# Performance work log

Hardware: AMD Instinct MI355X
Metric: run time of the kernel (lower is better)

## Reference

```python
import jax, jax.numpy as jnp
import numpy as np

ALPHA = 300.0   # attractor_alpha
N_ATT = 16      # n_attractors
MIN_D = 0.001
MAX_D = 10.0


def _resize_bilinear_ac(x, out_h, out_w):
    """Bilinear resize with align_corners=True on trailing (H, W) dims of [B,C,h,w]."""
    h, w = x.shape[-2], x.shape[-1]
    ys = jnp.arange(out_h, dtype=jnp.float32) * ((h - 1) / max(out_h - 1, 1))
    xs = jnp.arange(out_w, dtype=jnp.float32) * ((w - 1) / max(out_w - 1, 1))
    y0 = jnp.floor(ys).astype(jnp.int32); y1 = jnp.minimum(y0 + 1, h - 1)
    x0 = jnp.floor(xs).astype(jnp.int32); x1 = jnp.minimum(x0 + 1, w - 1)
    wy = (ys - y0.astype(jnp.float32))[:, None]   # [out_h, 1]
    wx = (xs - x0.astype(jnp.float32))[None, :]   # [1, out_w]
    v00 = x[..., y0[:, None], x0[None, :]]
    v01 = x[..., y0[:, None], x1[None, :]]
    v10 = x[..., y1[:, None], x0[None, :]]
    v11 = x[..., y1[:, None], x1[None, :]]
    top = v00 * (1 - wx) + v01 * wx
    bot = v10 * (1 - wx) + v11 * wx
    return top * (1 - wy) + bot * wy


def setup_inputs() -> dict:
    key = jax.random.key(0)
    k = jax.random.split(key, 7)
    B, C, H, W = 4, 128, 192, 192
    n_bins = 64
    x = jax.random.normal(k[0], (B, C, H, W), dtype=jnp.float32)
    prev_bin = jax.random.uniform(k[1], (B, n_bins, H // 2, W // 2), dtype=jnp.float32)
    prev_bin_embedding = jax.random.normal(k[2], (B, C, H // 2, W // 2), dtype=jnp.float32)
    w1 = jax.random.normal(k[3], (128, 128), dtype=jnp.float32) * 0.05
    b1 = jnp.zeros((128,), dtype=jnp.float32)
    w2 = jax.random.normal(k[4], (2 * N_ATT, 128), dtype=jnp.float32) * 0.05
    b2 = jnp.zeros((2 * N_ATT,), dtype=jnp.float32)
    return {"x": x, "prev_bin": prev_bin, "prev_bin_embedding": prev_bin_embedding,
            "w1": w1, "b1": b1, "w2": w2, "b2": b2}


def reference(x, prev_bin, prev_bin_embedding, w1, b1, w2, b2):
    B, C, H, W = x.shape
    # add (interpolated) previous bin embedding
    pe = _resize_bilinear_ac(prev_bin_embedding, H, W)
    h = x + pe
    # per-pixel MLP (two 1x1 convs)
    h = jax.nn.relu(jnp.einsum('bchw,oc->bohw', h, w1) + b1[:, None, None])
    att = jax.nn.relu(jnp.einsum('bchw,oc->bohw', h, w2) + b2[:, None, None]) + 0.001
    # [B, n_attractors, 2, H, W] -> take normed attractor points
    att = att.reshape(B, N_ATT, 2, H, W)[:, :, 0]          # [B, nA, H, W]
    # upsample previous bin centers to feature resolution
    bc = _resize_bilinear_ac(prev_bin, H, W)               # [B, nB, H, W]
    # broadcast-subtract + inverse attractor + mean over attractors
    dx = att[:, :, None, :, :] - bc[:, None, :, :, :]      # [B, nA, nB, H, W]
    delta_c = jnp.mean(dx / (1.0 + ALPHA * dx * dx), axis=1)  # gamma = 2
    bin_new_centers = bc + delta_c
    bin_centers = (MAX_D - MIN_D) * bin_new_centers + MIN_D
    bin_centers = jnp.clip(jnp.sort(bin_centers, axis=1), MIN_D, MAX_D)
    return bin_new_centers, bin_centers
```

## Files before the change

kernel.cpp:

```cpp
#include <hip/hip_runtime.h>

constexpr int Bc = 4, Cc = 128, Hc = 192, Wc = 192;
constexpr int HI = 96, WI = 96;
constexpr int NB = 64;
constexpr int NA = 16;
constexpr float SCL = 95.0f / 191.0f;

typedef __attribute__((ext_vector_type(8))) short bf16x8;
typedef __attribute__((ext_vector_type(4))) float f32x4;

__device__ __forceinline__ unsigned short f2bf(float f) {
  unsigned u = __builtin_bit_cast(unsigned, f);
  unsigned r = (u + 0x7FFFu + ((u >> 16) & 1u)) >> 16;
  return (unsigned short)r;
}
__device__ __forceinline__ float rcp_fast(float r) {
#if defined(__has_builtin)
#if __has_builtin(__builtin_amdgcn_rcpf)
  return __builtin_amdgcn_rcpf(r);
#else
  return 1.0f / r;
#endif
#else
  return 1.0f / r;
#endif
}

__global__ __launch_bounds__(256) void k_prep(
    const float* __restrict__ w1, const float* __restrict__ w2,
    unsigned short* __restrict__ w1p, unsigned short* __restrict__ w2p)
{
  const int t = blockIdx.x * 256 + threadIdx.x;
  if (t < 16384) {
    const int e  = t & 7;
    const int l  = (t >> 3) & 63;
    const int kt = (t >> 9) & 3;
    const int nt = t >> 11;
    const int n  = nt * 16 + (l & 15);
    const int k  = kt * 32 + (l >> 4) * 8 + e;
    w1p[t] = f2bf(w1[n * 128 + k]);
  } else {
    const int u  = t - 16384;
    const int e  = u & 7;
    const int l  = (u >> 3) & 63;
    const int kt = u >> 9;
    const int n  = 2 * (l & 15);
    const int k  = kt * 32 + (l >> 4) * 8 + e;
    w2p[u] = f2bf(w2[n * 128 + k]);
  }
}

__global__ __launch_bounds__(256, 3) void k_att(
    const float* __restrict__ x, const float* __restrict__ pbe,
    const unsigned short* __restrict__ w1p, const float* __restrict__ b1,
    const unsigned short* __restrict__ w2p, const float* __restrict__ b2,
    float* __restrict__ att)
{
  constexpr int PH = 136;
  constexpr int RP = 37;
  __shared__ __align__(16) unsigned char smem[32768 + 128 * RP * 4];
  unsigned short* w1_s  = (unsigned short*)smem;
  float*          row_s = (float*)(smem + 32768);
  unsigned short* a1_s  = (unsigned short*)(smem + 32768);

  const int tid = threadIdx.x;
  const int xg0 = blockIdx.x * 64;
  const int y = blockIdx.y;
  const int b = blockIdx.z;

  const float ysf = y * SCL;
  const int y0 = (int)ysf;
  const int y1 = min(y0 + 1, HI - 1);
  const float wy = ysf - (float)y0;
  const int xi0 = (int)(xg0 * SCL);

  const int lane = tid & 63;
  const int wv = tid >> 6;
  const int ln = lane & 15;
  const int qd = lane >> 4;
  const int m0 = wv * 16;

  const int px = m0 + ln;
  const int xg = xg0 + px;
  const float xsf = (float)xg * SCL;
  const int x0i = (int)xsf;
  const float wx = xsf - (float)x0i;
  const int xl = x0i - xi0;

  float4 wstage[8];
  {
    const float4* wp4 = (const float4*)w1p;
    #pragma unroll
    for (int i = 0; i < 8; ++i) wstage[i] = wp4[tid + 256 * i];
  }

  bf16x8 b2f[4];
  #pragma unroll
  for (int kt = 0; kt < 4; ++kt)
    b2f[kt] = *(const bf16x8*)&w2p[kt * 512 + lane * 8];
  float bias1[8];
  #pragma unroll
  for (int nt = 0; nt < 8; ++nt) bias1[nt] = b1[nt * 16 + ln];
  const float bias2 = b2[2 * ln];

  float xr[32];
  #pragma unroll
  for (int kt = 0; kt < 4; ++kt) {
    #pragma unroll
    for (int j = 0; j < 8; ++j) {
      const int c = kt * 32 + qd * 8 + j;
      xr[kt * 8 + j] = x[((size_t)(b * Cc + c) * Hc + y) * Wc + xg];
    }
  }

  #pragma unroll
  for (int i = 0; i < 18; ++i) {
    const int f = tid + 256 * i;
    const int c = f / 36;
    const int xi = f - c * 36;
    const int xgl = min(xi0 + xi, WI - 1);
    const float* p = pbe + (size_t)(b * Cc + c) * (HI * WI);
    const float top = p[y0 * WI + xgl];
    const float bot = p[y1 * WI + xgl];
    row_s[c * RP + xi] = top + wy * (bot - top);
  }

  {
    float4* ws4 = (float4*)w1_s;
    #pragma unroll
    for (int i = 0; i < 8; ++i) ws4[tid + 256 * i] = wstage[i];
  }
  __syncthreads();

  bf16x8 af[4];
  #pragma unroll
  for (int kt = 0; kt < 4; ++kt) {
    #pragma unroll
    for (int j = 0; j < 8; ++j) {
      const int c = kt * 32 + qd * 8 + j;
      const float v0 = row_s[c * RP + xl];
      const float v1 = row_s[c * RP + xl + 1];
      af[kt][j] = (short)f2bf(xr[kt * 8 + j] + v0 + wx * (v1 - v0));
    }
  }
  __syncthreads();

  f32x4 acc[8];
  #pragma unroll
  for (int nt = 0; nt < 8; ++nt) acc[nt] = f32x4{0.f, 0.f, 0.f, 0.f};
  #pragma unroll
  for (int nt = 0; nt < 8; ++nt) {
    #pragma unroll
    for (int kt = 0; kt < 4; ++kt) {
      const bf16x8 bf = *(const bf16x8*)&w1_s[(nt * 4 + kt) * 512 + lane * 8];
      acc[nt] = __builtin_amdgcn_mfma_f32_16x16x32_bf16(af[kt], bf, acc[nt], 0, 0, 0);
    }
  }

  #pragma unroll
  for (int nt = 0; nt < 8; ++nt) {
    const int n = nt * 16 + ln;
    const float bias = bias1[nt];
    #pragma unroll
    for (int r = 0; r < 4; ++r) {
      const int m = m0 + qd * 4 + r;
      a1_s[m * PH + n] = f2bf(fmaxf(acc[nt][r] + bias, 0.f));
    }
  }

  f32x4 acc2 = f32x4{0.f, 0.f, 0.f, 0.f};
  #pragma unroll
  for (int kt = 0; kt < 4; ++kt) {
    const bf16x8 a2 = *(const bf16x8*)&a1_s[(m0 + ln) * PH + kt * 32 + qd * 8];
    acc2 = __builtin_amdgcn_mfma_f32_16x16x32_bf16(a2, b2f[kt], acc2, 0, 0, 0);
  }
  #pragma unroll
  for (int r = 0; r < 4; ++r) {
    const int opx = m0 + qd * 4 + r;
    const float v = fmaxf(acc2[r] + bias2, 0.f) + 0.001f;
    att[((size_t)((b * Hc + y) * Wc) + xg0 + opx) * NA + ln] = v;
  }
}

__global__ __launch_bounds__(384, 4) void k_bins(
    const float* __restrict__ pb, const float* __restrict__ att,
    float* __restrict__ out0, float* __restrict__ out1)
{
  __shared__ __align__(16) float row_s[NB][WI];
  float* xch = &row_s[0][0];

  const int tid = threadIdx.x;
  const int h = (tid >= 192) ? 1 : 0;
  const int px = tid - 192 * h;
  const int y = blockIdx.x;
  const int b = blockIdx.y;

  const float ysf = y * SCL;
  const int y0 = (int)ysf;
  const int y1 = min(y0 + 1, HI - 1);
  const float wy = ysf - (float)y0;

  float am[16];
  {
    const float4* ap = (const float4*)(att + ((size_t)((b * Hc + y) * Wc) + px) * NA);
    const float4 a0 = ap[0], a1 = ap[1], a2 = ap[2], a3 = ap[3];
    am[0] = a0.x;  am[1] = a0.y;  am[2] = a0.z;  am[3] = a0.w;
    am[4] = a1.x;  am[5] = a1.y;  am[6] = a1.z;  am[7] = a1.w;
    am[8] = a2.x;  am[9] = a2.y;  am[10] = a2.z; am[11] = a2.w;
    am[12] = a3.x; am[13] = a3.y; am[14] = a3.z; am[15] = a3.w;
  }

  #pragma unroll
  for (int i = 0; i < 4; ++i) {
    const int u = tid + 384 * i;
    const int k = u / 24;
    const int g = u - k * 24;
    const float* base = pb + (size_t)(b * NB + k) * (HI * WI);
    const float4 t4 = *(const float4*)&base[y0 * WI + g * 4];
    const float4 b4 = *(const float4*)&base[y1 * WI + g * 4];
    float4 r;
    r.x = t4.x + wy * (b4.x - t4.x);
    r.y = t4.y + wy * (b4.y - t4.y);
    r.z = t4.z + wy * (b4.z - t4.z);
    r.w = t4.w + wy * (b4.w - t4.w);
    *(float4*)&row_s[k][g * 4] = r;
  }
  __syncthreads();

  const float xsf = px * SCL;
  const int x0 = (int)xsf;
  const float wx = xsf - (float)x0;

  const size_t obase = (size_t)(b * NB) * (Hc * Wc) + (size_t)y * Wc + px;
  float v[32];

  #pragma unroll
  for (int kb = 0; kb < 32; kb += 4) {
    float bc[4], dl[4];
    #pragma unroll
    for (int q = 0; q < 4; ++q) {
      const int k = h * 32 + kb + q;
      const float v0 = row_s[k][x0], v1 = row_s[k][x0 + 1];
      bc[q] = v0 + wx * (v1 - v0);
      dl[q] = 0.f;
    }
    #pragma unroll
    for (int j = 0; j < NA; ++j) {
      const float a = am[j];
      #pragma unroll
      for (int q = 0; q < 4; ++q) {
        const float d = a - bc[q];
        const float rq = fmaf(300.f * d, d, 1.f);
        dl[q] = fmaf(d, rcp_fast(rq), dl[q]);
      }
    }
    #pragma unroll
    for (int q = 0; q < 4; ++q) {
      const float bnc = fmaf(dl[q], 1.f / 16.f, bc[q]);
      out0[obase + (size_t)(h * 32 + kb + q) * (Hc * Wc)] = bnc;
      v[kb + q] = fmaf(9.999f, bnc, 0.001f);
    }
  }

  if (h == 0) {
    #pragma unroll
    for (int size = 2; size <= 32; size <<= 1)
      #pragma unroll
      for (int stride = size >> 1; stride >= 1; stride >>= 1)
        #pragma unroll
        for (int i = 0; i < 32; ++i)
          if ((i & stride) == 0) {
            const int j = i | stride;
            const bool asc = ((i & size) == 0);
            const float a = v[i], c = v[j];
            const float lo = fminf(a, c), hi = fmaxf(a, c);
            v[i] = asc ? lo : hi;
            v[j] = asc ? hi : lo;
          }
  } else {
    #pragma unroll
    for (int size = 2; size <= 32; size <<= 1)
      #pragma unroll
      for (int stride = size >> 1; stride >= 1; stride >>= 1)
        #pragma unroll
        for (int i = 0; i < 32; ++i)
          if ((i & stride) == 0) {
            const int j = i | stride;
            const bool asc = ((i & size) != 0);
            const float a = v[i], c = v[j];
            const float lo = fminf(a, c), hi = fmaxf(a, c);
            v[i] = asc ? lo : hi;
            v[j] = asc ? hi : lo;
          }
  }

  __syncthreads();
  if (h) {
    #pragma unroll
    for (int i = 0; i < 32; ++i) xch[i * 192 + px] = v[i];
  }
  __syncthreads();
  if (!h) {
    #pragma unroll
    for (int i = 0; i < 32; ++i) {
      const float o = xch[i * 192 + px];
      const float mn = fminf(v[i], o), mx = fmaxf(v[i], o);
      v[i] = mn;
      xch[i * 192 + px] = mx;
    }
  }
  __syncthreads();
  if (h) {
    #pragma unroll
    for (int i = 0; i < 32; ++i) v[i] = xch[i * 192 + px];
  }

  #pragma unroll
  for (int stride = 16; stride >= 1; stride >>= 1)
    #pragma unroll
    for (int i = 0; i < 32; ++i)
      if ((i & stride) == 0) {
        const int j = i | stride;
        const float a = v[i], c = v[j];
        v[i] = fminf(a, c);
        v[j] = fmaxf(a, c);
      }

  #pragma unroll
  for (int i = 0; i < 32; ++i) {
    out1[obase + (size_t)(h * 32 + i) * (Hc * Wc)] =
        fminf(fmaxf(v[i], 0.001f), 10.0f);
  }
}

extern "C" void kernel_launch(void* const* d_in, const int* in_sizes, int n_in,
                              void* d_out, int out_size, void* d_ws, size_t ws_size,
                              hipStream_t stream) {
  const float* x   = (const float*)d_in[0];
  const float* pb  = (const float*)d_in[1];
  const float* pbe = (const float*)d_in[2];
  const float* w1  = (const float*)d_in[3];
  const float* b1  = (const float*)d_in[4];
  const float* w2  = (const float*)d_in[5];
  const float* b2  = (const float*)d_in[6];

  float* out0 = (float*)d_out;
  float* out1 = out0 + (size_t)Bc * NB * Hc * Wc;

  unsigned short* w1p = (unsigned short*)d_ws;
  unsigned short* w2p = w1p + 16384;
  float* att = (float*)((char*)d_ws + 65536);

  k_prep<<<72, 256, 0, stream>>>(w1, w2, w1p, w2p);

  dim3 g1(Wc / 64, Hc, Bc);
  k_att<<<g1, 256, 0, stream>>>(x, pbe, w1p, b1, w2p, b2, att);

  dim3 g2(Hc, Bc);
  k_bins<<<g2, 384, 0, stream>>>(pb, att, out0, out1);
}
```

Before: 213.0 us.

## Fuse attractor MLP and bin-center kernels into one per-row kernel

Merges the attractor MLP kernel and the bin update kernel into a single kernel with one 384-thread block per image row. Attractor values now stay in shared memory instead of being written to and read back from a global workspace. The block covers the full row, so the interpolated embedding row is staged once in shared memory with an XOR swizzle to avoid bank conflicts. The trade-offs are a large 80KB shared allocation that limits occupancy, fewer blocks overall (768), and the MLP and bin phases running serially inside each block.

```diff
diff --git a/kernel.cpp b/kernel.cpp
--- a/kernel.cpp
+++ b/kernel.cpp
@@ -50,48 +50,44 @@
   }
 }
 
-__global__ __launch_bounds__(256, 3) void k_att(
+__global__ __launch_bounds__(384, 3) void k_row(
     const float* __restrict__ x, const float* __restrict__ pbe,
     const unsigned short* __restrict__ w1p, const float* __restrict__ b1,
     const unsigned short* __restrict__ w2p, const float* __restrict__ b2,
-    float* __restrict__ att)
+    const float* __restrict__ pb,
+    float* __restrict__ out0, float* __restrict__ out1)
 {
-  constexpr int PH = 136;
-  constexpr int RP = 37;
-  __shared__ __align__(16) unsigned char smem[32768 + 128 * RP * 4];
+  __shared__ __align__(16) unsigned char smem[81920];
   unsigned short* w1_s  = (unsigned short*)smem;
   float*          row_s = (float*)(smem + 32768);
-  unsigned short* a1_s  = (unsigned short*)(smem + 32768);
+  unsigned short* a1_b  = (unsigned short*)(smem + 32768);
+  float*          att_s = (float*)(smem + 58880);
+  float*          pbrow = (float*)smem;
+  float*          xch   = (float*)(smem + 24576);
 
   const int tid = threadIdx.x;
-  const int xg0 = blockIdx.x * 64;
-  const int y = blockIdx.y;
-  const int b = blockIdx.z;
+  const int y = blockIdx.x;
+  const int b = blockIdx.y;
+
+  const int lane = tid & 63;
+  const int wv = tid >> 6;
+  const int ln = lane & 15;
+  const int qd = lane >> 4;
 
   const float ysf = y * SCL;
   const int y0 = (int)ysf;
   const int y1 = min(y0 + 1, HI - 1);
   const float wy = ysf - (float)y0;
-  const int xi0 = (int)(xg0 * SCL);
-
-  const int lane = tid & 63;
-  const int wv = tid >> 6;
-  const int ln = lane & 15;
-  const int qd = lane >> 4;
-  const int m0 = wv * 16;
-
-  const int px = m0 + ln;
-  const int xg = xg0 + px;
-  const float xsf = (float)xg * SCL;
-  const int x0i = (int)xsf;
-  const float wx = xsf - (float)x0i;
-  const int xl = x0i - xi0;
-
-  float4 wstage[8];
+
+
+  float4 wstage[6];
   {
     const float4* wp4 = (const float4*)w1p;
     #pragma unroll
-    for (int i = 0; i < 8; ++i) wstage[i] = wp4[tid + 256 * i];
+    for (int i = 0; i < 6; ++i) {
+      const int u = tid + 384 * i;
+      wstage[i] = (u < 2048) ? wp4[u] : float4{0.f, 0.f, 0.f, 0.f};
+    }
   }
 
   bf16x8 b2f[4];
@@ -103,111 +99,114 @@
   for (int nt = 0; nt < 8; ++nt) bias1[nt] = b1[nt * 16 + ln];
   const float bias2 = b2[2 * ln];
 
-  float xr[32];
-  #pragma unroll
-  for (int kt = 0; kt < 4; ++kt) {
-    #pragma unroll
-    for (int j = 0; j < 8; ++j) {
-      const int c = kt * 32 + qd * 8 + j;
-      xr[kt * 8 + j] = x[((size_t)(b * Cc + c) * Hc + y) * Wc + xg];
-    }
-  }
-
-  #pragma unroll
-  for (int i = 0; i < 18; ++i) {
-    const int f = tid + 256 * i;
-    const int c = f / 36;
-    const int xi = f - c * 36;
-    const int xgl = min(xi0 + xi, WI - 1);
+  float xr[2][32];
+  #pragma unroll
+  for (int mt = 0; mt < 2; ++mt) {
+    const int px = wv * 32 + mt * 16 + ln;
+    #pragma unroll
+    for (int kt = 0; kt < 4; ++kt) {
+      #pragma unroll
+      for (int j = 0; j < 8; ++j) {
+        const int c = kt * 32 + qd * 8 + j;
+        xr[mt][kt * 8 + j] = x[((size_t)(b * Cc + c) * Hc + y) * Wc + px];
+      }
+    }
+  }
+
+  #pragma unroll
+  for (int i = 0; i < 32; ++i) {
+    const int f = tid + 384 * i;
+    const int c = f / 96;
+    const int xi = f - c * 96;
     const float* p = pbe + (size_t)(b * Cc + c) * (HI * WI);
-    const float top = p[y0 * WI + xgl];
-    const float bot = p[y1 * WI + xgl];
-    row_s[c * RP + xi] = top + wy * (bot - top);
+    const float top = p[y0 * WI + xi];
+    const float bot = p[y1 * WI + xi];
+    row_s[c * 96 + (xi ^ ((((c >> 3) & 3)) << 3))] = top + wy * (bot - top);
   }
 
   {
     float4* ws4 = (float4*)w1_s;
     #pragma unroll
-    for (int i = 0; i < 8; ++i) ws4[tid + 256 * i] = wstage[i];
-  }
-  __syncthreads();
-
-  bf16x8 af[4];
-  #pragma unroll
-  for (int kt = 0; kt < 4; ++kt) {
-    #pragma unroll
-    for (int j = 0; j < 8; ++j) {
-      const int c = kt * 32 + qd * 8 + j;
-      const float v0 = row_s[c * RP + xl];
-      const float v1 = row_s[c * RP + xl + 1];
-      af[kt][j] = (short)f2bf(xr[kt * 8 + j] + v0 + wx * (v1 - v0));
-    }
-  }
-  __syncthreads();
-
-  f32x4 acc[8];
-  #pragma unroll
-  for (int nt = 0; nt < 8; ++nt) acc[nt] = f32x4{0.f, 0.f, 0.f, 0.f};
-  #pragma unroll
-  for (int nt = 0; nt < 8; ++nt) {
+    for (int i = 0; i < 6; ++i) {
+      const int u = tid + 384 * i;
+      if (u < 2048) ws4[u] = wstage[i];
+    }
+  }
+  __syncthreads();
+
+  bf16x8 af[2][4];
+  const int sw = qd << 3;
+  #pragma unroll
+  for (int mt = 0; mt < 2; ++mt) {
+    const int px = wv * 32 + mt * 16 + ln;
+    const float xsf = (float)px * SCL;
+    const int xl = (int)xsf;
+    const float wx = xsf - (float)xl;
+    const int i0 = xl ^ sw;
+    const int i1 = (xl + 1) ^ sw;
     #pragma unroll
     for (int kt = 0; kt < 4; ++kt) {
-      const bf16x8 bf = *(const bf16x8*)&w1_s[(nt * 4 + kt) * 512 + lane * 8];
-      acc[nt] = __builtin_amdgcn_mfma_f32_16x16x32_bf16(af[kt], bf, acc[nt], 0, 0, 0);
-    }
-  }
-
-  #pragma unroll
-  for (int nt = 0; nt < 8; ++nt) {
-    const int n = nt * 16 + ln;
-    const float bias = bias1[nt];
+      #pragma unroll
+      for (int j = 0; j < 8; ++j) {
+        const int c = kt * 32 + qd * 8 + j;
+        const float v0 = row_s[c * 96 + i0];
+        const float v1 = row_s[c * 96 + i1];
+        af[mt][kt][j] = (short)f2bf(xr[mt][kt * 8 + j] + v0 + wx * (v1 - v0));
+      }
+    }
+  }
+  __syncthreads();
+
+  unsigned short* a1w = a1_b + wv * (16 * 136);
+
+  #pragma unroll
+  for (int mt = 0; mt < 2; ++mt) {
+    f32x4 acc[8];
+    #pragma unroll
+    for (int nt = 0; nt < 8; ++nt) acc[nt] = f32x4{0.f, 0.f, 0.f, 0.f};
+    #pragma unroll
+    for (int nt = 0; nt < 8; ++nt) {
+      #pragma unroll
+      for (int kt = 0; kt < 4; ++kt) {
+        const bf16x8 bf = *(const bf16x8*)&w1_s[(nt * 4 + kt) * 512 + lane * 8];
+        acc[nt] = __builtin_amdgcn_mfma_f32_16x16x32_bf16(af[mt][kt], bf, acc[nt], 0, 0, 0);
+      }
+    }
+    #pragma unroll
+    for (int nt = 0; nt < 8; ++nt) {
+      const int n = nt * 16 + ln;
+      const float bias = bias1[nt];
+      #pragma unroll
+      for (int r = 0; r < 4; ++r) {
+        a1w[(qd * 4 + r) * 136 + n] = f2bf(fmaxf(acc[nt][r] + bias, 0.f));
+      }
+    }
+    f32x4 acc2 = f32x4{0.f, 0.f, 0.f, 0.f};
+    #pragma unroll
+    for (int kt = 0; kt < 4; ++kt) {
+      const bf16x8 a2 = *(const bf16x8*)&a1w[ln * 136 + kt * 32 + qd * 8];
+      acc2 = __builtin_amdgcn_mfma_f32_16x16x32_bf16(a2, b2f[kt], acc2, 0, 0, 0);
+    }
     #pragma unroll
     for (int r = 0; r < 4; ++r) {
-      const int m = m0 + qd * 4 + r;
-      a1_s[m * PH + n] = f2bf(fmaxf(acc[nt][r] + bias, 0.f));
-    }
-  }
-
-  f32x4 acc2 = f32x4{0.f, 0.f, 0.f, 0.f};
-  #pragma unroll
-  for (int kt = 0; kt < 4; ++kt) {
-    const bf16x8 a2 = *(const bf16x8*)&a1_s[(m0 + ln) * PH + kt * 32 + qd * 8];
-    acc2 = __builtin_amdgcn_mfma_f32_16x16x32_bf16(a2, b2f[kt], acc2, 0, 0, 0);
-  }
-  #pragma unroll
-  for (int r = 0; r < 4; ++r) {
-    const int opx = m0 + qd * 4 + r;
-    const float v = fmaxf(acc2[r] + bias2, 0.f) + 0.001f;
-    att[((size_t)((b * Hc + y) * Wc) + xg0 + opx) * NA + ln] = v;
-  }
-}
-
-__global__ __launch_bounds__(384, 4) void k_bins(
-    const float* __restrict__ pb, const float* __restrict__ att,
-    float* __restrict__ out0, float* __restrict__ out1)
-{
-  __shared__ __align__(16) float row_s[NB][WI];
-  float* xch = &row_s[0][0];
-
-  const int tid = threadIdx.x;
+      const int opx = wv * 32 + mt * 16 + qd * 4 + r;
+      att_s[opx * 20 + ln] = fmaxf(acc2[r] + bias2, 0.f) + 0.001f;
+    }
+  }
+  __syncthreads();
+
+
   const int h = (tid >= 192) ? 1 : 0;
   const int px = tid - 192 * h;
-  const int y = blockIdx.x;
-  const int b = blockIdx.y;
-
-  const float ysf = y * SCL;
-  const int y0 = (int)ysf;
-  const int y1 = min(y0 + 1, HI - 1);
-  const float wy = ysf - (float)y0;
 
   float am[16];
   {
-    const float4* ap = (const float4*)(att + ((size_t)((b * Hc + y) * Wc) + px) * NA);
-    const float4 a0 = ap[0], a1 = ap[1], a2 = ap[2], a3 = ap[3];
-    am[0] = a0.x;  am[1] = a0.y;  am[2] = a0.z;  am[3] = a0.w;
-    am[4] = a1.x;  am[5] = a1.y;  am[6] = a1.z;  am[7] = a1.w;
-    am[8] = a2.x;  am[9] = a2.y;  am[10] = a2.z; am[11] = a2.w;
-    am[12] = a3.x; am[13] = a3.y; am[14] = a3.z; am[15] = a3.w;
+    const f32x4* ap = (const f32x4*)&att_s[px * 20];
+    const f32x4 a0 = ap[0], a1 = ap[1], a2 = ap[2], a3 = ap[3];
+    am[0] = a0[0];  am[1] = a0[1];  am[2] = a0[2];  am[3] = a0[3];
+    am[4] = a1[0];  am[5] = a1[1];  am[6] = a1[2];  am[7] = a1[3];
+    am[8] = a2[0];  am[9] = a2[1];  am[10] = a2[2]; am[11] = a2[3];
+    am[12] = a3[0]; am[13] = a3[1]; am[14] = a3[2]; am[15] = a3[3];
   }
 
   #pragma unroll
@@ -223,7 +222,7 @@
     r.y = t4.y + wy * (b4.y - t4.y);
     r.z = t4.z + wy * (b4.z - t4.z);
     r.w = t4.w + wy * (b4.w - t4.w);
-    *(float4*)&row_s[k][g * 4] = r;
+    *(float4*)&pbrow[k * 96 + g * 4] = r;
   }
   __syncthreads();
 
@@ -240,7 +239,7 @@
     #pragma unroll
     for (int q = 0; q < 4; ++q) {
       const int k = h * 32 + kb + q;
-      const float v0 = row_s[k][x0], v1 = row_s[k][x0 + 1];
+      const float v0 = pbrow[k * 96 + x0], v1 = pbrow[k * 96 + x0 + 1];
       bc[q] = v0 + wx * (v1 - v0);
       dl[q] = 0.f;
     }
@@ -349,13 +348,9 @@
 
   unsigned short* w1p = (unsigned short*)d_ws;
   unsigned short* w2p = w1p + 16384;
-  float* att = (float*)((char*)d_ws + 65536);
 
   k_prep<<<72, 256, 0, stream>>>(w1, w2, w1p, w2p);
 
-  dim3 g1(Wc / 64, Hc, Bc);
-  k_att<<<g1, 256, 0, stream>>>(x, pbe, w1p, b1, w2p, b2, att);
-
-  dim3 g2(Hc, Bc);
-  k_bins<<<g2, 384, 0, stream>>>(pb, att, out0, out1);
-}
+  dim3 g(Hc, Bc);
+  k_row<<<g, 384, 0, stream>>>(x, pbe, w1p, b1, w2p, b2, pb, out0, out1);
+}
```

New measurement: 265.7 us. 1.25x slower.

## Halve k_att weight staging in LDS and split k_bins rows across two blocks

Applied to the files above, without the earlier changes.

k_att now loads the first-layer weights into shared memory in two halves. The first half is used for four output tiles, then overwritten with the second half. This halves the weight buffer and raises the launch-bounds occupancy target from 3 to 4 blocks, at the cost of an extra barrier and more phases. k_bins now splits each row into two 192-thread blocks, each covering 96 pixels with a narrower padded interpolation buffer. This gives more, smaller blocks for better SM fill and lower LDS use per block. The bitonic sort's two direction branches are merged into one loop with a direction predicate.

```diff
diff --git a/kernel.cpp b/kernel.cpp
--- a/kernel.cpp
+++ b/kernel.cpp
@@ -50,7 +50,7 @@
   }
 }
 
-__global__ __launch_bounds__(256, 3) void k_att(
+__global__ __launch_bounds__(256, 4) void k_att(
     const float* __restrict__ x, const float* __restrict__ pbe,
     const unsigned short* __restrict__ w1p, const float* __restrict__ b1,
     const unsigned short* __restrict__ w2p, const float* __restrict__ b2,
@@ -58,10 +58,10 @@
 {
   constexpr int PH = 136;
   constexpr int RP = 37;
-  __shared__ __align__(16) unsigned char smem[32768 + 128 * RP * 4];
+  __shared__ __align__(16) unsigned char smem[16384 + 128 * RP * 4];
   unsigned short* w1_s  = (unsigned short*)smem;
-  float*          row_s = (float*)(smem + 32768);
-  unsigned short* a1_s  = (unsigned short*)(smem + 32768);
+  float*          row_s = (float*)(smem + 16384);
+  unsigned short* a1_s  = (unsigned short*)(smem + 16384);
 
   const int tid = threadIdx.x;
   const int xg0 = blockIdx.x * 64;
@@ -80,28 +80,18 @@
   const int qd = lane >> 4;
   const int m0 = wv * 16;
 
-  const int px = m0 + ln;
-  const int xg = xg0 + px;
+  const int xg = xg0 + m0 + ln;
   const float xsf = (float)xg * SCL;
   const int x0i = (int)xsf;
   const float wx = xsf - (float)x0i;
   const int xl = x0i - xi0;
 
-  float4 wstage[8];
+  float4 wstageA[4];
   {
     const float4* wp4 = (const float4*)w1p;
     #pragma unroll
-    for (int i = 0; i < 8; ++i) wstage[i] = wp4[tid + 256 * i];
-  }
-
-  bf16x8 b2f[4];
-  #pragma unroll
-  for (int kt = 0; kt < 4; ++kt)
-    b2f[kt] = *(const bf16x8*)&w2p[kt * 512 + lane * 8];
-  float bias1[8];
-  #pragma unroll
-  for (int nt = 0; nt < 8; ++nt) bias1[nt] = b1[nt * 16 + ln];
-  const float bias2 = b2[2 * ln];
+    for (int i = 0; i < 4; ++i) wstageA[i] = wp4[tid + 256 * i];
+  }
 
   float xr[32];
   #pragma unroll
@@ -128,7 +118,7 @@
   {
     float4* ws4 = (float4*)w1_s;
     #pragma unroll
-    for (int i = 0; i < 8; ++i) ws4[tid + 256 * i] = wstage[i];
+    for (int i = 0; i < 4; ++i) ws4[tid + 256 * i] = wstageA[i];
   }
   __syncthreads();
 
@@ -145,20 +135,61 @@
   }
   __syncthreads();
 
+  float4 wstageB[4];
+  {
+    const float4* wp4 = (const float4*)w1p;
+    #pragma unroll
+    for (int i = 0; i < 4; ++i) wstageB[i] = wp4[1024 + tid + 256 * i];
+  }
+  float bias1[8];
+  #pragma unroll
+  for (int nt = 0; nt < 8; ++nt) bias1[nt] = b1[nt * 16 + ln];
+
   f32x4 acc[8];
   #pragma unroll
   for (int nt = 0; nt < 8; ++nt) acc[nt] = f32x4{0.f, 0.f, 0.f, 0.f};
   #pragma unroll
-  for (int nt = 0; nt < 8; ++nt) {
+  for (int nt = 0; nt < 4; ++nt) {
     #pragma unroll
     for (int kt = 0; kt < 4; ++kt) {
       const bf16x8 bf = *(const bf16x8*)&w1_s[(nt * 4 + kt) * 512 + lane * 8];
       acc[nt] = __builtin_amdgcn_mfma_f32_16x16x32_bf16(af[kt], bf, acc[nt], 0, 0, 0);
     }
   }
-
-  #pragma unroll
-  for (int nt = 0; nt < 8; ++nt) {
+  #pragma unroll
+  for (int nt = 0; nt < 4; ++nt) {
+    const int n = nt * 16 + ln;
+    const float bias = bias1[nt];
+    #pragma unroll
+    for (int r = 0; r < 4; ++r) {
+      const int m = m0 + qd * 4 + r;
+      a1_s[m * PH + n] = f2bf(fmaxf(acc[nt][r] + bias, 0.f));
+    }
+  }
+  __syncthreads();
+
+  {
+    float4* ws4 = (float4*)w1_s;
+    #pragma unroll
+    for (int i = 0; i < 4; ++i) ws4[tid + 256 * i] = wstageB[i];
+  }
+  bf16x8 b2f[4];
+  #pragma unroll
+  for (int kt = 0; kt < 4; ++kt)
+    b2f[kt] = *(const bf16x8*)&w2p[kt * 512 + lane * 8];
+  const float bias2 = b2[2 * ln];
+  __syncthreads();
+
+  #pragma unroll
+  for (int nt = 4; nt < 8; ++nt) {
+    #pragma unroll
+    for (int kt = 0; kt < 4; ++kt) {
+      const bf16x8 bf = *(const bf16x8*)&w1_s[((nt - 4) * 4 + kt) * 512 + lane * 8];
+      acc[nt] = __builtin_amdgcn_mfma_f32_16x16x32_bf16(af[kt], bf, acc[nt], 0, 0, 0);
+    }
+  }
+  #pragma unroll
+  for (int nt = 4; nt < 8; ++nt) {
     const int n = nt * 16 + ln;
     const float bias = bias1[nt];
     #pragma unroll
@@ -182,23 +213,30 @@
   }
 }
 
-__global__ __launch_bounds__(384, 4) void k_bins(
+__global__ __launch_bounds__(192, 6) void k_bins(
     const float* __restrict__ pb, const float* __restrict__ att,
     float* __restrict__ out0, float* __restrict__ out1)
 {
-  __shared__ __align__(16) float row_s[NB][WI];
-  float* xch = &row_s[0][0];
+  constexpr int PW = 51;
+  __shared__ __align__(16) float smem2[NB * PW];
+  float* pbrow = smem2;
+  float* xch   = smem2;
 
   const int tid = threadIdx.x;
-  const int h = (tid >= 192) ? 1 : 0;
-  const int px = tid - 192 * h;
-  const int y = blockIdx.x;
-  const int b = blockIdx.y;
+  const int y  = blockIdx.x;
+  const int b  = blockIdx.y;
+  const int hx = blockIdx.z;
+
+  const int h  = (tid >= 96) ? 1 : 0;
+  const int p  = tid - 96 * h;
+  const int px = 96 * hx + p;
 
   const float ysf = y * SCL;
   const int y0 = (int)ysf;
   const int y1 = min(y0 + 1, HI - 1);
   const float wy = ysf - (float)y0;
+
+  const int xi0 = hx ? 47 : 0;
 
   float am[16];
   {
@@ -211,25 +249,24 @@
   }
 
   #pragma unroll
-  for (int i = 0; i < 4; ++i) {
-    const int u = tid + 384 * i;
-    const int k = u / 24;
-    const int g = u - k * 24;
-    const float* base = pb + (size_t)(b * NB + k) * (HI * WI);
-    const float4 t4 = *(const float4*)&base[y0 * WI + g * 4];
-    const float4 b4 = *(const float4*)&base[y1 * WI + g * 4];
-    float4 r;
-    r.x = t4.x + wy * (b4.x - t4.x);
-    r.y = t4.y + wy * (b4.y - t4.y);
-    r.z = t4.z + wy * (b4.z - t4.z);
-    r.w = t4.w + wy * (b4.w - t4.w);
-    *(float4*)&row_s[k][g * 4] = r;
+  for (int i = 0; i < 17; ++i) {
+    const int u = tid + 192 * i;
+    if (u < 3200) {
+      const int k = u / 50;
+      const int xi = u - k * 50;
+      const int xs = min(xi0 + xi, WI - 1);
+      const float* base = pb + (size_t)(b * NB + k) * (HI * WI);
+      const float top = base[y0 * WI + xs];
+      const float bot = base[y1 * WI + xs];
+      pbrow[k * PW + xi] = top + wy * (bot - top);
+    }
   }
   __syncthreads();
 
   const float xsf = px * SCL;
   const int x0 = (int)xsf;
   const float wx = xsf - (float)x0;
+  const int xl = x0 - xi0;
 
   const size_t obase = (size_t)(b * NB) * (Hc * Wc) + (size_t)y * Wc + px;
   float v[32];
@@ -240,7 +277,7 @@
     #pragma unroll
     for (int q = 0; q < 4; ++q) {
       const int k = h * 32 + kb + q;
-      const float v0 = row_s[k][x0], v1 = row_s[k][x0 + 1];
+      const float v0 = pbrow[k * PW + xl], v1 = pbrow[k * PW + xl + 1];
       bc[q] = v0 + wx * (v1 - v0);
       dl[q] = 0.f;
     }
@@ -262,69 +299,57 @@
     }
   }
 
-  if (h == 0) {
-    #pragma unroll
-    for (int size = 2; size <= 32; size <<= 1)
+  #pragma unroll
+  for (int size = 2; size <= 32; size <<= 1) {
+    #pragma unroll
+    for (int stride = size >> 1; stride >= 1; stride >>= 1) {
       #pragma unroll
-      for (int stride = size >> 1; stride >= 1; stride >>= 1)
-        #pragma unroll
-        for (int i = 0; i < 32; ++i)
-          if ((i & stride) == 0) {
-            const int j = i | stride;
-            const bool asc = ((i & size) == 0);
-            const float a = v[i], c = v[j];
-            const float lo = fminf(a, c), hi = fmaxf(a, c);
-            v[i] = asc ? lo : hi;
-            v[j] = asc ? hi : lo;
-          }
-  } else {
-    #pragma unroll
-    for (int size = 2; size <= 32; size <<= 1)
-      #pragma unroll
-      for (int stride = size >> 1; stride >= 1; stride >>= 1)
-        #pragma unroll
-        for (int i = 0; i < 32; ++i)
-          if ((i & stride) == 0) {
-            const int j = i | stride;
-            const bool asc = ((i & size) != 0);
-            const float a = v[i], c = v[j];
-            const float lo = fminf(a, c), hi = fmaxf(a, c);
-            v[i] = asc ? lo : hi;
-            v[j] = asc ? hi : lo;
-          }
+      for (int i = 0; i < 32; ++i) {
+        if ((i & stride) == 0) {
+          const int j = i | stride;
+          const bool asc = (((i & size) == 0) != (h == 1));
+          const float a = v[i], c = v[j];
+          const float lo = fminf(a, c), hi = fmaxf(a, c);
+          v[i] = asc ? lo : hi;
+          v[j] = asc ? hi : lo;
+        }
+      }
+    }
   }
 
   __syncthreads();
   if (h) {
     #pragma unroll
-    for (int i = 0; i < 32; ++i) xch[i * 192 + px] = v[i];
+    for (int i = 0; i < 32; ++i) xch[i * 96 + p] = v[i];
   }
   __syncthreads();
   if (!h) {
     #pragma unroll
     for (int i = 0; i < 32; ++i) {
-      const float o = xch[i * 192 + px];
+      const float o = xch[i * 96 + p];
       const float mn = fminf(v[i], o), mx = fmaxf(v[i], o);
       v[i] = mn;
-      xch[i * 192 + px] = mx;
+      xch[i * 96 + p] = mx;
     }
   }
   __syncthreads();
   if (h) {
     #pragma unroll
-    for (int i = 0; i < 32; ++i) v[i] = xch[i * 192 + px];
-  }
-
-  #pragma unroll
-  for (int stride = 16; stride >= 1; stride >>= 1)
-    #pragma unroll
-    for (int i = 0; i < 32; ++i)
+    for (int i = 0; i < 32; ++i) v[i] = xch[i * 96 + p];
+  }
+
+  #pragma unroll
+  for (int stride = 16; stride >= 1; stride >>= 1) {
+    #pragma unroll
+    for (int i = 0; i < 32; ++i) {
       if ((i & stride) == 0) {
         const int j = i | stride;
         const float a = v[i], c = v[j];
         v[i] = fminf(a, c);
         v[j] = fmaxf(a, c);
       }
+    }
+  }
 
   #pragma unroll
   for (int i = 0; i < 32; ++i) {
@@ -356,6 +381,6 @@
   dim3 g1(Wc / 64, Hc, Bc);
   k_att<<<g1, 256, 0, stream>>>(x, pbe, w1p, b1, w2p, b2, att);
 
-  dim3 g2(Hc, Bc);
-  k_bins<<<g2, 384, 0, stream>>>(pb, att, out0, out1);
-}
+  dim3 g2(Hc, Bc, 2);
+  k_bins<<<g2, 192, 0, stream>>>(pb, att, out0, out1);
+}
```

After: 235.6 us. 1.11x slower.
